# Optimization experiments

Hardware: AMD Instinct MI355X
Metric: run time of the kernel (lower is better)

Reference implementation:

```python
import jax, jax.numpy as jnp
import numpy as np

B, V, L, C = 4, 8, 256, 1024
H, O = 16, 4
Dh = C // H
NEG = -1e9

def setup_inputs() -> dict:
    key = jax.random.key(0)
    ks = jax.random.split(key, 16)
    inp = {}
    inp['v'] = jax.random.normal(ks[0], (B, V, L, C), jnp.float32)
    inp['k'] = jax.random.normal(ks[1], (B, V, L, C), jnp.float32)
    inp['q'] = jax.random.normal(ks[2], (B, V, L, C), jnp.float32)
    inp['masks'] = jax.random.uniform(ks[3], (O, B, V, 1, 1, L)) < 0.15  # True = masked out
    inp['tau'] = jnp.ones((1,), jnp.float32)
    inp['training'] = 1
    u = jax.random.uniform(ks[4], (B, V, O), jnp.float32, minval=1e-20, maxval=1.0)
    inp['gumbel_noise'] = -jnp.log(-jnp.log(u))  # standard Gumbel, = -log(Exp(1))
    s = 1.0 / np.sqrt(C)
    inp['Wv'] = jax.random.normal(ks[5], (C, C), jnp.float32) * s
    inp['bv'] = jnp.zeros((C,), jnp.float32)
    inp['Wk'] = jax.random.normal(ks[6], (C, C), jnp.float32) * s
    inp['bk'] = jnp.zeros((C,), jnp.float32)
    inp['Wq'] = jax.random.normal(ks[7], (C, C), jnp.float32) * s
    inp['bq'] = jnp.zeros((C,), jnp.float32)
    inp['Wm'] = jax.random.normal(ks[8], (C, C), jnp.float32) * s
    inp['bm'] = jnp.zeros((C,), jnp.float32)
    inp['W1'] = jax.random.normal(ks[9], (C, C // 2), jnp.float32) * s
    inp['W2'] = jax.random.normal(ks[10], (C // 2, O), jnp.float32) * (1.0 / np.sqrt(C // 2))
    inp['b2'] = jnp.zeros((O,), jnp.float32)
    return inp


def reference(v, k, q, masks, tau, training, gumbel_noise,
              Wv, bv, Wk, bk, Wq, bq, Wm, bm, W1, W2, b2):
    # --- HardRoutingBlock (pooling='avg'): avg-pool over seq, MLP, gumbel-softmax ---
    pooled = jnp.mean(v, axis=2)                          # [B,V,C]
    h = jax.nn.relu(pooled @ W1)                          # [B,V,C/2]
    logits = h @ W2 + b2                                  # [B,V,O]
    logp = jax.nn.log_softmax(logits, axis=-1)
    alphas = jax.nn.softmax((logp + gumbel_noise) / tau[0], axis=-1)  # [B,V,O]

    # --- multi-head projections: [B,V,L,C] -> [B,V,H,L,Dh] ---
    def split_heads(x):
        return x.reshape(B, V, L, H, Dh).transpose(0, 1, 3, 2, 4)
    vv = split_heads(v @ Wv + bv)
    kk = split_heads(k @ Wk + bk)
    qq = split_heads(q @ Wq + bq)

    scores = jnp.einsum('bvhqd,bvhkd->bvhqk', qq, kk) / np.sqrt(Dh)  # [B,V,H,L,L]
    # per-order masked softmax: masks [O,B,V,1,1,L]
    att = jax.nn.softmax(jnp.where(masks, NEG, scores[None]), axis=-1)  # [O,B,V,H,L,L]
    # routed combination: einsum('bvl,bvlcnm->bvcnm') with l=orders
    att_map = jnp.einsum('bvo,obvhqk->bvhqk', alphas, att)
    atted = jnp.einsum('bvhqk,bvhkd->bvhqd', att_map, vv)  # [B,V,H,L,Dh]
    atted = atted.transpose(0, 1, 3, 2, 4).reshape(B, V, L, C)
    return atted @ Wm + bm
```

## Files before the change

### kernel.cpp

```cpp
#include <hip/hip_runtime.h>

#define B_   4
#define V_   8
#define L_   256
#define C_   1024
#define H_   16
#define O_   4
#define DH_  64
#define BV_  32
#define M_   8192
#define MB_  (1024 * 1024)

typedef short bf16x8 __attribute__((ext_vector_type(8)));
typedef short bf16x4 __attribute__((ext_vector_type(4)));
typedef float f32x4  __attribute__((ext_vector_type(4)));
typedef float f32x16 __attribute__((ext_vector_type(16)));

__device__ __forceinline__ float bflo(unsigned int w) { return __uint_as_float(w << 16); }
__device__ __forceinline__ float bfhi(unsigned int w) { return __uint_as_float(w & 0xffff0000u); }
__device__ __forceinline__ unsigned int f2bfbits(float f) {
    unsigned int i = __float_as_uint(f);
    return (i + 0x7fffu + ((i >> 16) & 1u)) >> 16;
}
__device__ __forceinline__ unsigned int packbf(float a, float b) {
    return f2bfbits(a) | (f2bfbits(b) << 16);
}
__device__ __forceinline__ unsigned int cvtpk_bf16(float lo, float hi) {
    unsigned int r;
    asm("v_cvt_pk_bf16_f32 %0, %1, %2" : "=v"(r) : "v"(lo), "v"(hi));
    return r;
}

typedef const __attribute__((address_space(1))) unsigned int* gas_t;
typedef __attribute__((address_space(3))) unsigned int* las_t;
__device__ __forceinline__ void gll16(const void* g, void* l) {
    __builtin_amdgcn_global_load_lds((gas_t)g, (las_t)l, 16, 0, 0);
}

__device__ __forceinline__ void conv_body(const float* __restrict__ in,
                                          unsigned short* __restrict__ outp,
                                          int blk, int t)
{
    const size_t i = ((size_t)blk * 256 + t) * 8;
    const float4 f0 = *(const float4*)(in + i);
    const float4 f1 = *(const float4*)(in + i + 4);
    uint4 o;
    o.x = packbf(f0.x, f0.y); o.y = packbf(f0.z, f0.w);
    o.z = packbf(f1.x, f1.y); o.w = packbf(f1.z, f1.w);
    *(uint4*)(outp + i) = o;
}

__device__ __forceinline__ void pools_body(const float* __restrict__ v,
                                           float* __restrict__ pbuf2,
                                           int pb, int t)
{
    const int bv = pb >> 3, lc = pb & 7;
    const float* vb = v + (size_t)bv * (L_ * C_) + (size_t)lc * 32 * C_ + t * 4;
    float a0 = 0.f, a1 = 0.f, a2 = 0.f, a3 = 0.f;
#pragma unroll
    for (int l = 0; l < 32; ++l) {
        const float4 f = *(const float4*)(vb + (size_t)l * C_);
        a0 += f.x; a1 += f.y; a2 += f.z; a3 += f.w;
    }
    float4 o; o.x = a0; o.y = a1; o.z = a2; o.w = a3;
    *(float4*)(pbuf2 + ((size_t)lc * 32 + bv) * C_ + t * 4) = o;
}

__device__ __forceinline__ void wprep_body(const float* __restrict__ W,
                                           unsigned short* __restrict__ Wt,
                                           float (*tile)[65], int k0, int n0, int t)
{
    const int r = t >> 2, c4 = (t & 3) * 16;
#pragma unroll
    for (int i = 0; i < 4; ++i) {
        const float4 f = *(const float4*)(W + (size_t)(k0 + r) * C_ + n0 + c4 + i * 4);
        tile[r][c4 + i * 4 + 0] = f.x; tile[r][c4 + i * 4 + 1] = f.y;
        tile[r][c4 + i * 4 + 2] = f.z; tile[r][c4 + i * 4 + 3] = f.w;
    }
    __syncthreads();
    unsigned int ow[8];
#pragma unroll
    for (int p = 0; p < 8; ++p)
        ow[p] = packbf(tile[c4 + 2 * p][r], tile[c4 + 2 * p + 1][r]);
    unsigned short* dst = Wt + (size_t)(n0 + r) * C_ + k0 + c4;
    uint4 o0; o0.x = ow[0]; o0.y = ow[1]; o0.z = ow[2]; o0.w = ow[3];
    uint4 o1; o1.x = ow[4]; o1.y = ow[5]; o1.z = ow[6]; o1.w = ow[7];
    *(uint4*)dst = o0;
    *(uint4*)(dst + 8) = o1;
}

__global__ __launch_bounds__(256) void conv_k(const float* __restrict__ in,
                                              unsigned short* __restrict__ outp)
{ conv_body(in, outp, blockIdx.x, threadIdx.x); }

__global__ __launch_bounds__(256) void pools_k(const float* __restrict__ v,
                                               float* __restrict__ pbuf2)
{ pools_body(v, pbuf2, blockIdx.x, threadIdx.x); }

__global__ __launch_bounds__(256) void wprep_k(const float* __restrict__ W,
                                               unsigned short* __restrict__ Wt)
{
    __shared__ float tile[64][65];
    wprep_body(W, Wt, tile, blockIdx.x * 64, blockIdx.y * 64, threadIdx.x);
}

__global__ __launch_bounds__(1024) void maskpack_k(
    const void* __restrict__ src, unsigned char* __restrict__ dst)
{
    __shared__ int v_word;
    const int t = threadIdx.x;
    if (t == 0) v_word = 1;
    __syncthreads();
    const unsigned int* s32 = (const unsigned int*)src;
    const unsigned int w = s32[t];
    if (w > 1u && w != 0x3F800000u) atomicAnd(&v_word, 0);
    __syncthreads();
    const bool word_mode = (v_word != 0);
    const unsigned char* s8 = (const unsigned char*)src;
#pragma unroll
    for (int i = 0; i < 8; ++i) {
        const int idx = t * 8 + i;
        const int bv = idx >> 8, l = idx & 255;
        unsigned int bits = 0;
#pragma unroll
        for (int o = 0; o < O_; ++o) {
            const int mi = (o * BV_ + bv) * L_ + l;
            const unsigned int m = word_mode ? (s32[mi] != 0u) : (s8[mi] != 0);
            bits |= m << o;
        }
        dst[idx] = (unsigned char)bits;
    }
}

__global__ __launch_bounds__(256) void prep_k(
    const float* __restrict__ q, const float* __restrict__ k, const float* __restrict__ v,
    const void* __restrict__ msk,
    const float* __restrict__ Wq, const float* __restrict__ Wk,
    const float* __restrict__ Wv, const float* __restrict__ Wm,
    unsigned short* __restrict__ cq, unsigned short* __restrict__ ck,
    unsigned short* __restrict__ cv,
    float* __restrict__ pbuf2, unsigned char* __restrict__ mpk,
    unsigned short* __restrict__ Wtb)
{
    __shared__ float tile[64][65];
    const int blk = blockIdx.x;
    const int t = threadIdx.x;
    if (blk < 12288) {
        const int wsel = blk >> 12;
        const float* in = (wsel == 0) ? q : (wsel == 1) ? k : v;
        unsigned short* outp = (wsel == 0) ? cq : (wsel == 1) ? ck : cv;
        conv_body(in, outp, blk & 4095, t);
    } else if (blk < 12544) {
        pools_body(v, pbuf2, blk - 12288, t);
    } else if (blk < 12548) {
        __shared__ int v_word;
        if (t == 0) v_word = 1;
        __syncthreads();
        const unsigned int* s32 = (const unsigned int*)msk;
        const unsigned int w = s32[t];
        if (w > 1u && w != 0x3F800000u) atomicAnd(&v_word, 0);
        __syncthreads();
        const bool word_mode = (v_word != 0);
        const unsigned char* s8 = (const unsigned char*)msk;
        const int tt = (blk - 12544) * 256 + t;
#pragma unroll
        for (int i = 0; i < 8; ++i) {
            const int idx = tt * 8 + i;
            const int bv = idx >> 8, l = idx & 255;
            unsigned int bits = 0;
#pragma unroll
            for (int o = 0; o < O_; ++o) {
                const int mi = (o * BV_ + bv) * L_ + l;
                const unsigned int m = word_mode ? (s32[mi] != 0u) : (s8[mi] != 0);
                bits |= m << o;
            }
            mpk[idx] = (unsigned char)bits;
        }
    } else {
        const int wb = blk - 12548;
        const int wsel = wb >> 8;
        const float* W = (wsel == 0) ? Wq : (wsel == 1) ? Wk : (wsel == 2) ? Wv : Wm;
        unsigned short* Wt = Wtb + (size_t)wsel * (C_ * C_);
        const int b = wb & 255;
        wprep_body(W, Wt, tile, (b & 15) * 64, (b >> 4) * 64, t);
    }
}

__global__ __launch_bounds__(256) void poolr_k(const float* __restrict__ pbuf2,
                                               float* __restrict__ pooled)
{
    const int idx = blockIdx.x * 256 + threadIdx.x;
    float s = 0.f;
#pragma unroll
    for (int p = 0; p < 8; ++p) s += pbuf2[(size_t)p * (32 * C_) + idx];
    pooled[idx] = s * (1.0f / 256.0f);
}

__global__ __launch_bounds__(256) void mlp1_k(const float* __restrict__ pooled,
                                              const float* __restrict__ W1,
                                              float* __restrict__ pbuf)
{
    const int t = threadIdx.x;
    const int col = blockIdx.x * 32 + (t & 31);
    const int b0 = (t >> 5) * 4;
    const int c0 = blockIdx.y * 32;
    float a0 = 0.f, a1 = 0.f, a2 = 0.f, a3 = 0.f;
#pragma unroll
    for (int c = c0; c < c0 + 32; ++c) {
        const float wv = W1[(size_t)c * 512 + col];
        a0 = fmaf(pooled[(size_t)(b0 + 0) * C_ + c], wv, a0);
        a1 = fmaf(pooled[(size_t)(b0 + 1) * C_ + c], wv, a1);
        a2 = fmaf(pooled[(size_t)(b0 + 2) * C_ + c], wv, a2);
        a3 = fmaf(pooled[(size_t)(b0 + 3) * C_ + c], wv, a3);
    }
    const size_t pb = ((size_t)blockIdx.y * 32 + b0) * 512 + col;
    pbuf[pb]        = a0;
    pbuf[pb + 512]  = a1;
    pbuf[pb + 1024] = a2;
    pbuf[pb + 1536] = a3;
}

__global__ __launch_bounds__(256) void mlp2_k(const float* __restrict__ pbuf,
                                              const float* __restrict__ W2,
                                              const float* __restrict__ b2,
                                              const float* __restrict__ gum,
                                              const float* __restrict__ tau,
                                              float* __restrict__ alphas)
{
    __shared__ float red[4][O_];
    const int bv = blockIdx.x, t = threadIdx.x;
    float h0 = 0.f, h1 = 0.f;
#pragma unroll
    for (int ch = 0; ch < 32; ++ch) {
        h0 += pbuf[((size_t)ch * 32 + bv) * 512 + t];
        h1 += pbuf[((size_t)ch * 32 + bv) * 512 + 256 + t];
    }
    h0 = fmaxf(h0, 0.f); h1 = fmaxf(h1, 0.f);
    float part[O_];
#pragma unroll
    for (int o = 0; o < O_; ++o)
        part[o] = h0 * W2[t * O_ + o] + h1 * W2[(t + 256) * O_ + o];
#pragma unroll
    for (int off = 32; off >= 1; off >>= 1) {
#pragma unroll
        for (int o = 0; o < O_; ++o) part[o] += __shfl_down(part[o], off, 64);
    }
    const int wid = t >> 6, lane = t & 63;
    if (lane == 0) {
#pragma unroll
        for (int o = 0; o < O_; ++o) red[wid][o] = part[o];
    }
    __syncthreads();
    if (t == 0) {
        float lg[O_];
#pragma unroll
        for (int o = 0; o < O_; ++o)
            lg[o] = red[0][o] + red[1][o] + red[2][o] + red[3][o] + b2[o];
        float mx = fmaxf(fmaxf(lg[0], lg[1]), fmaxf(lg[2], lg[3]));
        float s = 0.f;
#pragma unroll
        for (int o = 0; o < O_; ++o) s += expf(lg[o] - mx);
        const float lse = logf(s) + mx;
        const float it = 1.0f / tau[0];
        float y[O_];
#pragma unroll
        for (int o = 0; o < O_; ++o) y[o] = (lg[o] - lse + gum[bv * O_ + o]) * it;
        float my = fmaxf(fmaxf(y[0], y[1]), fmaxf(y[2], y[3]));
        float z = 0.f;
#pragma unroll
        for (int o = 0; o < O_; ++o) { y[o] = expf(y[o] - my); z += y[o]; }
        const float iz = 1.0f / z;
#pragma unroll
        for (int o = 0; o < O_; ++o) alphas[bv * O_ + o] = y[o] * iz;
    }
}

template <bool PROJSTORE>
__device__ __forceinline__ void mgemm_body(
    const unsigned short* __restrict__ Ab, const unsigned short* __restrict__ Wt,
    const float* __restrict__ bias, void* __restrict__ out_, int n0, int m0)
{
    __shared__ unsigned short As[128][64];
    __shared__ unsigned short Bs[128][64];
    const int t = threadIdx.x;
    const int w = t >> 6, lane = t & 63;
    const int wm = (w >> 1) * 64, wn = (w & 1) * 64;
    const int fr = lane & 15;
    const int fq = lane >> 4;

    const int sr = w * 8 + (lane >> 3);
    const int sc = ((lane & 7) ^ ((lane >> 3) & 7)) * 8;
    const unsigned short* aP = Ab + (size_t)(m0 + sr) * C_ + sc;
    const unsigned short* bP = Wt + (size_t)(n0 + sr) * C_ + sc;

    const int frm = (fr & 7);

    f32x4 acc[4][4] = {};

    for (int kt = 0; kt < C_; kt += 64) {
        __syncthreads();
#pragma unroll
        for (int i = 0; i < 4; ++i) {
            gll16(aP + (size_t)i * 32 * C_ + kt, &As[i * 32 + w * 8][0]);
            gll16(bP + (size_t)i * 32 * C_ + kt, &Bs[i * 32 + w * 8][0]);
        }
        __syncthreads();

#pragma unroll
        for (int c = 0; c < 2; ++c) {
            const int rk = ((c * 4 + fq) ^ frm) * 8;
            bf16x8 af[4], bfr[4];
#pragma unroll
            for (int i = 0; i < 4; ++i)
                af[i] = *(const bf16x8*)&As[wm + i * 16 + fr][rk];
#pragma unroll
            for (int j = 0; j < 4; ++j)
                bfr[j] = *(const bf16x8*)&Bs[wn + j * 16 + fr][rk];
#pragma unroll
            for (int i = 0; i < 4; ++i)
#pragma unroll
                for (int j = 0; j < 4; ++j)
                    acc[i][j] = __builtin_amdgcn_mfma_f32_16x16x32_bf16(af[i], bfr[j], acc[i][j], 0, 0, 0);
        }
    }

#pragma unroll
    for (int j = 0; j < 4; ++j) {
        const int gcol = n0 + wn + j * 16 + fr;
        const float bj = bias[gcol];
#pragma unroll
        for (int i = 0; i < 4; ++i) {
#pragma unroll
            for (int r = 0; r < 4; ++r) {
                const int grow = m0 + wm + i * 16 + fq * 4 + r;
                const float val = acc[i][j][r] + bj;
                if (PROJSTORE) {
                    const int bvb = grow >> 8, l = grow & 255;
                    const int hh = gcol >> 6, dh = gcol & 63;
                    ((unsigned short*)out_)[(((size_t)bvb * H_ + hh) * L_ + l) * DH_ + dh] =
                        (unsigned short)f2bfbits(val);
                } else {
                    ((float*)out_)[(size_t)grow * C_ + gcol] = val;
                }
            }
        }
    }
}

template <bool PROJSTORE>
__global__ __launch_bounds__(256) void mgemm_k(
    const unsigned short* __restrict__ Ab, const unsigned short* __restrict__ Wt,
    const float* __restrict__ bias, void* __restrict__ out_)
{
    mgemm_body<PROJSTORE>(Ab, Wt, bias, out_, blockIdx.x * 128, blockIdx.y * 128);
}

__global__ __launch_bounds__(256) void mgemm3_k(
    const unsigned short* __restrict__ cq, const unsigned short* __restrict__ ck,
    const unsigned short* __restrict__ cv, const unsigned short* __restrict__ Wtb,
    const float* __restrict__ bq, const float* __restrict__ bk, const float* __restrict__ bvv,
    unsigned short* __restrict__ qqw, unsigned short* __restrict__ kkw,
    unsigned short* __restrict__ vvw)
{
    const int b = blockIdx.x;
    const int swz = (b & 7) * 192 + (b >> 3);
    const int which = swz >> 9;
    const int g = swz & 511;
    const unsigned short* A = (which == 0) ? cq : (which == 1) ? ck : cv;
    const unsigned short* W = Wtb + (size_t)which * (C_ * C_);
    const float* bias = (which == 0) ? bq : (which == 1) ? bk : bvv;
    unsigned short* outp = (which == 0) ? qqw : (which == 1) ? kkw : vvw;
    mgemm_body<true>(A, W, bias, (void*)outp, (g & 7) * 128, (g >> 3) * 128);
}

__global__ __launch_bounds__(256) void mgemmf_k(
    const unsigned short* __restrict__ Ab, const unsigned short* __restrict__ Wt,
    const float* __restrict__ bias, float* __restrict__ out_)
{
    const int b = blockIdx.x;
    const int swz = (b & 7) * 64 + (b >> 3);
    mgemm_body<false>(Ab, Wt, bias, (void*)out_, (swz & 7) * 128, (swz >> 3) * 128);
}

__global__ __launch_bounds__(256) void attn_k(
    const unsigned short* __restrict__ qq, const unsigned short* __restrict__ kk,
    const unsigned short* __restrict__ vv, const unsigned char* __restrict__ mpk,
    const float* __restrict__ alphas, unsigned short* __restrict__ atted)
{
    __shared__ unsigned short Vt[DH_][260];
    __shared__ unsigned int mkw[64];
    __shared__ float al[O_];
    const int h = blockIdx.x, bv = blockIdx.y;
    const int t = threadIdx.x;
    const int w = t >> 6, lane = t & 63;
    const int fr = lane & 31, hf = lane >> 5;
    const size_t hb = ((size_t)bv * H_ + h) * (L_ * DH_);

    {
        const uint4* gv = (const uint4*)(vv + hb + (size_t)t * DH_);
#pragma unroll
        for (int i = 0; i < 8; ++i) {
            const uint4 wv = gv[i];
            const unsigned int ws4[4] = {wv.x, wv.y, wv.z, wv.w};
#pragma unroll
            for (int jd = 0; jd < 4; ++jd) {
                Vt[i * 8 + jd * 2 + 0][t] = (unsigned short)(ws4[jd] & 0xffffu);
                Vt[i * 8 + jd * 2 + 1][t] = (unsigned short)(ws4[jd] >> 16);
            }
        }
    }
    if (t < 64) mkw[t] = ((const unsigned int*)mpk)[bv * 64 + t];
    if (t < O_) al[t] = alphas[bv * O_ + t];
    __syncthreads();
    const float al0 = al[0], al1 = al[1], al2 = al[2], al3 = al[3];

#pragma unroll 1
    for (int qt = 0; qt < 2; ++qt) {
        const int q32 = w * 64 + qt * 32;
        bf16x8 qf[4];
#pragma unroll
        for (int st = 0; st < 4; ++st)
            qf[st] = *(const bf16x8*)(qq + hb + (size_t)(q32 + fr) * DH_ + st * 16 + hf * 8);

        float T0 = 0.f, T1 = 0.f, T2 = 0.f, T3 = 0.f;
#pragma unroll 1
        for (int j = 0; j < 8; ++j) {
            bf16x8 kf[4];
#pragma unroll
            for (int st = 0; st < 4; ++st)
                kf[st] = *(const bf16x8*)(kk + hb + (size_t)(j * 32 + fr) * DH_ + st * 16 + hf * 8);
            f32x16 s = {};
#pragma unroll
            for (int st = 0; st < 4; ++st)
                s = __builtin_amdgcn_mfma_f32_32x32x16_bf16(kf[st], qf[st], s, 0, 0, 0);
#pragma unroll
            for (int c = 0; c < 4; ++c) {
                const unsigned int iv = (~mkw[j * 8 + c * 2 + hf]) & 0x0F0F0F0Fu;
#pragma unroll
                for (int r = 0; r < 4; ++r) {
                    const float e = __expf(s[c * 4 + r] * 0.125f);
                    const unsigned int nib = iv >> (r * 8);
                    T0 = fmaf(e, (float)( nib       & 1u), T0);
                    T1 = fmaf(e, (float)((nib >> 1) & 1u), T1);
                    T2 = fmaf(e, (float)((nib >> 2) & 1u), T2);
                    T3 = fmaf(e, (float)((nib >> 3) & 1u), T3);
                }
            }
        }
        T0 += __shfl_xor(T0, 32, 64);
        T1 += __shfl_xor(T1, 32, 64);
        T2 += __shfl_xor(T2, 32, 64);
        T3 += __shfl_xor(T3, 32, 64);
        const float c0 = al0 * __builtin_amdgcn_rcpf(fmaxf(T0, 1e-30f));
        const float c1 = al1 * __builtin_amdgcn_rcpf(fmaxf(T1, 1e-30f));
        const float c2 = al2 * __builtin_amdgcn_rcpf(fmaxf(T2, 1e-30f));
        const float c3 = al3 * __builtin_amdgcn_rcpf(fmaxf(T3, 1e-30f));

        f32x16 o0 = {};
        f32x16 o1 = {};
#pragma unroll 1
        for (int j = 0; j < 8; ++j) {
            bf16x8 kf[4];
#pragma unroll
            for (int st = 0; st < 4; ++st)
                kf[st] = *(const bf16x8*)(kk + hb + (size_t)(j * 32 + fr) * DH_ + st * 16 + hf * 8);
            f32x16 s = {};
#pragma unroll
            for (int st = 0; st < 4; ++st)
                s = __builtin_amdgcn_mfma_f32_32x32x16_bf16(kf[st], qf[st], s, 0, 0, 0);

            unsigned int pe[4][2];
#pragma unroll
            for (int c = 0; c < 4; ++c) {
                const unsigned int iv = (~mkw[j * 8 + c * 2 + hf]) & 0x0F0F0F0Fu;
                float p[4];
#pragma unroll
                for (int r = 0; r < 4; ++r) {
                    const float e = __expf(s[c * 4 + r] * 0.125f);
                    const unsigned int nib = iv >> (r * 8);
                    float cf =      c0 * (float)( nib       & 1u);
                    cf = fmaf(c1, (float)((nib >> 1) & 1u), cf);
                    cf = fmaf(c2, (float)((nib >> 2) & 1u), cf);
                    cf = fmaf(c3, (float)((nib >> 3) & 1u), cf);
                    p[r] = e * cf;
                }
                pe[c][0] = cvtpk_bf16(p[0], p[1]);
                pe[c][1] = cvtpk_bf16(p[2], p[3]);
            }
#pragma unroll
            for (int b = 0; b < 2; ++b) {
                const unsigned int qe0 = pe[2 * b][0],     qe1 = pe[2 * b][1];
                const unsigned int qo0 = pe[2 * b + 1][0], qo1 = pe[2 * b + 1][1];
                const unsigned int xe0 = (unsigned int)__shfl_xor((int)qe0, 32, 64);
                const unsigned int xe1 = (unsigned int)__shfl_xor((int)qe1, 32, 64);
                const unsigned int xo0 = (unsigned int)__shfl_xor((int)qo0, 32, 64);
                const unsigned int xo1 = (unsigned int)__shfl_xor((int)qo1, 32, 64);
                union { unsigned int d[4]; bf16x8 v; } pa;
                pa.d[0] = hf ? xo0 : qe0;
                pa.d[1] = hf ? xo1 : qe1;
                pa.d[2] = hf ? qo0 : xe0;
                pa.d[3] = hf ? qo1 : xe1;

                const int kc = j * 32 + b * 16 + hf * 8;
                union { struct { bf16x4 lo, hi; } p2; bf16x8 v; } v0u, v1u;
                v0u.p2.lo = *(const bf16x4*)&Vt[ 0 + fr][kc];
                v0u.p2.hi = *(const bf16x4*)&Vt[ 0 + fr][kc + 4];
                v1u.p2.lo = *(const bf16x4*)&Vt[32 + fr][kc];
                v1u.p2.hi = *(const bf16x4*)&Vt[32 + fr][kc + 4];
                o0 = __builtin_amdgcn_mfma_f32_32x32x16_bf16(pa.v, v0u.v, o0, 0, 0, 0);
                o1 = __builtin_amdgcn_mfma_f32_32x32x16_bf16(pa.v, v1u.v, o1, 0, 0, 0);
            }
        }
#pragma unroll
        for (int reg = 0; reg < 16; ++reg) {
            const int qrow = q32 + (reg & 3) + 8 * (reg >> 2) + 4 * hf;
            unsigned short* dst = atted + ((size_t)bv * L_ + qrow) * C_ + h * DH_;
            dst[fr]      = (unsigned short)f2bfbits(o0[reg]);
            dst[32 + fr] = (unsigned short)f2bfbits(o1[reg]);
        }
    }
}

extern "C" void kernel_launch(void* const* d_in, const int* in_sizes, int n_in,
                              void* d_out, int out_size, void* d_ws, size_t ws_size,
                              hipStream_t stream)
{
    (void)in_sizes; (void)n_in; (void)out_size;
    const float* v   = (const float*)d_in[0];
    const float* k   = (const float*)d_in[1];
    const float* q   = (const float*)d_in[2];
    const void*  msk = d_in[3];
    const float* tau = (const float*)d_in[4];
    const float* gum = (const float*)d_in[6];
    const float* Wv  = (const float*)d_in[7];
    const float* bvp = (const float*)d_in[8];
    const float* Wk  = (const float*)d_in[9];
    const float* bkp = (const float*)d_in[10];
    const float* Wq  = (const float*)d_in[11];
    const float* bqp = (const float*)d_in[12];
    const float* Wm  = (const float*)d_in[13];
    const float* bmp = (const float*)d_in[14];
    const float* W1  = (const float*)d_in[15];
    const float* W2  = (const float*)d_in[16];
    const float* b2  = (const float*)d_in[17];
    float* out = (float*)d_out;

    char* ws = (char*)d_ws;

    if (ws_size >= (size_t)128 * MB_) {
        float* alphas       = (float*)ws;
        unsigned char* mpk  = (unsigned char*)(ws + 1024);
        float* pooled       = (float*)(ws + 16384);
        float* pbuf2        = (float*)(ws + 147456);
        float* pbuf         = (float*)(ws + 1196032);
        unsigned short* Wtb = (unsigned short*)(ws + (size_t)4 * MB_);
        unsigned short* cq  = (unsigned short*)(ws + (size_t)14 * MB_);
        unsigned short* ck  = (unsigned short*)(ws + (size_t)30 * MB_);
        unsigned short* cv  = (unsigned short*)(ws + (size_t)46 * MB_);
        unsigned short* qqw = (unsigned short*)(ws + (size_t)62 * MB_);
        unsigned short* kkw = (unsigned short*)(ws + (size_t)78 * MB_);
        unsigned short* vvw = (unsigned short*)(ws + (size_t)94 * MB_);
        unsigned short* atw = (unsigned short*)(ws + (size_t)110 * MB_);

        hipLaunchKernelGGL(prep_k, dim3(13572), dim3(256), 0, stream,
                           q, k, v, msk, Wq, Wk, Wv, Wm, cq, ck, cv, pbuf2, mpk, Wtb);
        hipLaunchKernelGGL(poolr_k, dim3(128), dim3(256), 0, stream, pbuf2, pooled);
        hipLaunchKernelGGL(mlp1_k, dim3(16, 32), dim3(256), 0, stream, pooled, W1, pbuf);
        hipLaunchKernelGGL(mlp2_k, dim3(BV_), dim3(256), 0, stream,
                           pbuf, W2, b2, gum, tau, alphas);
        hipLaunchKernelGGL(mgemm3_k, dim3(1536), dim3(256), 0, stream,
                           cq, ck, cv, Wtb, bqp, bkp, bvp, qqw, kkw, vvw);
        hipLaunchKernelGGL(attn_k, dim3(H_, BV_), dim3(256), 0, stream,
                           qqw, kkw, vvw, mpk, alphas, atw);
        hipLaunchKernelGGL(mgemmf_k, dim3(512), dim3(256), 0, stream,
                           atw, Wtb + (size_t)3 * (C_ * C_), bmp, out);
    } else {
        float* alphas       = (float*)ws;
        unsigned char* mpk  = (unsigned char*)(ws + 1024);
        float* pooled       = (float*)(ws + 16384);
        float* pbuf2        = (float*)(ws + 147456);
        float* pbuf         = (float*)(ws + 1196032);
        unsigned short* Wt  = (unsigned short*)(ws + 16384);
        unsigned short* qqw = (unsigned short*)(ws + 2113536);
        unsigned short* kkw = qqw + (size_t)M_ * C_;
        unsigned short* vvw = kkw + (size_t)M_ * C_;
        unsigned short* atw = vvw + (size_t)M_ * C_;

        hipLaunchKernelGGL(pools_k, dim3(256), dim3(256), 0, stream, v, pbuf2);
        hipLaunchKernelGGL(poolr_k, dim3(128), dim3(256), 0, stream, pbuf2, pooled);
        hipLaunchKernelGGL(mlp1_k, dim3(16, 32), dim3(256), 0, stream, pooled, W1, pbuf);
        hipLaunchKernelGGL(mlp2_k, dim3(BV_), dim3(256), 0, stream,
                           pbuf, W2, b2, gum, tau, alphas);
        hipLaunchKernelGGL(maskpack_k, dim3(1), dim3(1024), 0, stream, msk, mpk);

        hipLaunchKernelGGL(conv_k, dim3(4096), dim3(256), 0, stream, q, atw);
        hipLaunchKernelGGL(wprep_k, dim3(16, 16), dim3(256), 0, stream, Wq, Wt);
        hipLaunchKernelGGL((mgemm_k<true>), dim3(8, 64), dim3(256), 0, stream,
                           atw, Wt, bqp, (void*)qqw);
        hipLaunchKernelGGL(conv_k, dim3(4096), dim3(256), 0, stream, k, atw);
        hipLaunchKernelGGL(wprep_k, dim3(16, 16), dim3(256), 0, stream, Wk, Wt);
        hipLaunchKernelGGL((mgemm_k<true>), dim3(8, 64), dim3(256), 0, stream,
                           atw, Wt, bkp, (void*)kkw);
        hipLaunchKernelGGL(conv_k, dim3(4096), dim3(256), 0, stream, v, atw);
        hipLaunchKernelGGL(wprep_k, dim3(16, 16), dim3(256), 0, stream, Wv, Wt);
        hipLaunchKernelGGL((mgemm_k<true>), dim3(8, 64), dim3(256), 0, stream,
                           atw, Wt, bvp, (void*)vvw);

        hipLaunchKernelGGL(attn_k, dim3(H_, BV_), dim3(256), 0, stream,
                           qqw, kkw, vvw, mpk, alphas, atw);

        hipLaunchKernelGGL(wprep_k, dim3(16, 16), dim3(256), 0, stream, Wm, Wt);
        hipLaunchKernelGGL((mgemm_k<false>), dim3(8, 64), dim3(256), 0, stream,
                           atw, Wt, bmp, (void*)out);
    }
}
```

Baseline: 185.9 us.

## Double-buffer LDS tiles in projection GEMM to overlap global loads with MFMA

Splits the GEMM shared-memory tiles into two ping-pong buffers and issues the next K-tile's direct-to-LDS loads before computing on the current one. Partial vmcnt waits plus raw barriers replace the load-then-sync loop, so global memory latency can hide behind MFMA work. LDS use doubles to 64KB per block, which may lower occupancy, and the hand-counted vmcnt values must match the number of outstanding loads to stay correct.

```diff
diff --git a/kernel.cpp b/kernel.cpp
--- a/kernel.cpp
+++ b/kernel.cpp
@@ -280,8 +280,8 @@
     const unsigned short* __restrict__ Ab, const unsigned short* __restrict__ Wt,
     const float* __restrict__ bias, void* __restrict__ out_, int n0, int m0)
 {
-    __shared__ unsigned short As[128][64];
-    __shared__ unsigned short Bs[128][64];
+    __shared__ unsigned short As0[128][64], As1[128][64];
+    __shared__ unsigned short Bs0[128][64], Bs1[128][64];
     const int t = threadIdx.x;
     const int w = t >> 6, lane = t & 63;
     const int wm = (w >> 1) * 64, wn = (w & 1) * 64;
@@ -297,32 +297,56 @@
 
     f32x4 acc[4][4] = {};
 
-    for (int kt = 0; kt < C_; kt += 64) {
-        __syncthreads();
-#pragma unroll
-        for (int i = 0; i < 4; ++i) {
-            gll16(aP + (size_t)i * 32 * C_ + kt, &As[i * 32 + w * 8][0]);
-            gll16(bP + (size_t)i * 32 * C_ + kt, &Bs[i * 32 + w * 8][0]);
-        }
-        __syncthreads();
-
-#pragma unroll
-        for (int c = 0; c < 2; ++c) {
-            const int rk = ((c * 4 + fq) ^ frm) * 8;
-            bf16x8 af[4], bfr[4];
-#pragma unroll
-            for (int i = 0; i < 4; ++i)
-                af[i] = *(const bf16x8*)&As[wm + i * 16 + fr][rk];
-#pragma unroll
-            for (int j = 0; j < 4; ++j)
-                bfr[j] = *(const bf16x8*)&Bs[wn + j * 16 + fr][rk];
-#pragma unroll
-            for (int i = 0; i < 4; ++i)
-#pragma unroll
-                for (int j = 0; j < 4; ++j)
-                    acc[i][j] = __builtin_amdgcn_mfma_f32_16x16x32_bf16(af[i], bfr[j], acc[i][j], 0, 0, 0);
-        }
-    }
+#define STAGE(AB, BB, KT)                                                   \
+    {                                                                       \
+        _Pragma("unroll")                                                   \
+        for (int i_ = 0; i_ < 4; ++i_) {                                    \
+            gll16(aP + (size_t)i_ * 32 * C_ + (KT), &AB[i_ * 32 + w * 8][0]);\
+            gll16(bP + (size_t)i_ * 32 * C_ + (KT), &BB[i_ * 32 + w * 8][0]);\
+        }                                                                   \
+    }
+
+#define COMPUTE(AB, BB)                                                     \
+    {                                                                       \
+        _Pragma("unroll")                                                   \
+        for (int c_ = 0; c_ < 2; ++c_) {                                    \
+            const int rk_ = ((c_ * 4 + fq) ^ frm) * 8;                      \
+            bf16x8 af_[4], bf_[4];                                          \
+            _Pragma("unroll")                                               \
+            for (int i_ = 0; i_ < 4; ++i_)                                  \
+                af_[i_] = *(const bf16x8*)&AB[wm + i_ * 16 + fr][rk_];      \
+            _Pragma("unroll")                                               \
+            for (int j_ = 0; j_ < 4; ++j_)                                  \
+                bf_[j_] = *(const bf16x8*)&BB[wn + j_ * 16 + fr][rk_];      \
+            _Pragma("unroll")                                               \
+            for (int i_ = 0; i_ < 4; ++i_)                                  \
+                _Pragma("unroll")                                           \
+                for (int j_ = 0; j_ < 4; ++j_)                              \
+                    acc[i_][j_] = __builtin_amdgcn_mfma_f32_16x16x32_bf16(  \
+                        af_[i_], bf_[j_], acc[i_][j_], 0, 0, 0);            \
+        }                                                                   \
+    }
+
+    STAGE(As0, Bs0, 0);
+#pragma unroll 1
+    for (int kt = 0; kt < C_; kt += 128) {
+        STAGE(As1, Bs1, kt + 64);
+        asm volatile("s_waitcnt vmcnt(8)" ::: "memory");
+        __builtin_amdgcn_s_barrier();
+        COMPUTE(As0, Bs0);
+        __builtin_amdgcn_s_barrier();
+        if (kt + 128 < C_) {
+            STAGE(As0, Bs0, kt + 128);
+            asm volatile("s_waitcnt vmcnt(8)" ::: "memory");
+        } else {
+            asm volatile("s_waitcnt vmcnt(0)" ::: "memory");
+        }
+        __builtin_amdgcn_s_barrier();
+        COMPUTE(As1, Bs1);
+        __builtin_amdgcn_s_barrier();
+    }
+#undef STAGE
+#undef COMPUTE
 
 #pragma unroll
     for (int j = 0; j < 4; ++j) {
```

New measurement: 183.7 us, median of 3. About the same (-1.2%).
